# Performance work log

Hardware: AMD Instinct MI355X
Metric: run time of the kernel (lower is better)

Reference implementation:

```python
import jax, jax.numpy as jnp
import numpy as np


def setup_inputs() -> dict:
    key = jax.random.key(0)
    ks = jax.random.split(key, 9)
    V, D, C, B = 100000, 128, 10, 16384
    return {
        "target_w_id": jax.random.randint(ks[0], (B,), 0, V),
        "context_w_ids": jax.random.randint(ks[1], (B, C), 0, V),
        "R": jax.random.normal(ks[2], (V, D), dtype=jnp.float32),
        "M_w": jax.random.normal(ks[3], (2 * D, 2 * D), dtype=jnp.float32) * 0.05,
        "M_b": jax.random.normal(ks[4], (2 * D,), dtype=jnp.float32) * 0.05,
        "U_w": jax.random.normal(ks[5], (D, 2 * D), dtype=jnp.float32) * 0.05,
        "U_b": jax.random.normal(ks[6], (D,), dtype=jnp.float32) * 0.05,
        "W_w": jax.random.normal(ks[7], (D, 2 * D), dtype=jnp.float32) * 0.05,
        "W_b": jax.random.normal(ks[8], (D,), dtype=jnp.float32) * 0.05,
    }


def reference(target_w_id, context_w_ids, R, M_w, M_b, U_w, U_b, W_w, W_b):
    # Gather embeddings: tw [B, D], cw [B, C, D]
    tw = R[target_w_id]
    cw = R[context_w_ids]
    B, C, D = cw.shape
    # Concat context embed with (broadcast) target embed -> [B, C, 2D]
    tw_b = jnp.broadcast_to(tw[:, None, :], (B, C, D))
    stacked = jnp.concatenate([cw, tw_b], axis=-1)
    # Linear M (torch: x @ W.T + b), ReLU, sum over context window -> h [B, 2D]
    proj = jnp.einsum("bcd,ed->bce", stacked, M_w) + M_b
    h = jnp.sum(jax.nn.relu(proj), axis=1)
    posterior_mu = h @ U_w.T + U_b
    posterior_sigma = jax.nn.softplus(h @ W_w.T + W_b)
    return (posterior_mu, posterior_sigma)
```

## Files before the change

kernel.cpp:

```cpp
#include <hip/hip_runtime.h>
#include <hip/hip_bf16.h>

typedef __attribute__((ext_vector_type(8))) short short8;
typedef __attribute__((ext_vector_type(4))) float floatx4;
typedef __attribute__((ext_vector_type(2))) float floatx2;

static __device__ __forceinline__ short f2bf(float f) {
    union { float f; unsigned u; } v; v.f = f;
    unsigned r = v.u + 0x7fffu + ((v.u >> 16) & 1u);
    return (short)(r >> 16);
}
static __device__ __forceinline__ float bf2f(short s) {
    union { unsigned u; float f; } v; v.u = ((unsigned)(unsigned short)s) << 16;
    return v.f;
}

#define C_CTX 10
#define D_EMB 128
#define E_DIM 256


__global__ void prep_main(const float* __restrict__ Mw, const float* __restrict__ Uw,
                          const float* __restrict__ Ww, short* __restrict__ M1f,
                          short* __restrict__ M2f, short* __restrict__ B2f)
{
    int u = blockIdx.x * 256 + threadIdx.x;
    if (u < 8192) {
        int f = u & 4095;
        int l = f & 63, kc = (f >> 6) & 3, grp = f >> 8;
        int e = grp * 16 + (l & 15);
        int k = kc * 32 + (l >> 4) * 8 + ((u < 4096) ? 0 : 128);
        const float* src = Mw + (size_t)e * E_DIM + k;
        float4 x = *(const float4*)src;
        float4 y = *(const float4*)(src + 4);
        short8 o;
        o[0]=f2bf(x.x); o[1]=f2bf(x.y); o[2]=f2bf(x.z); o[3]=f2bf(x.w);
        o[4]=f2bf(y.x); o[5]=f2bf(y.y); o[6]=f2bf(y.z); o[7]=f2bf(y.w);
        *(short8*)(((u < 4096) ? M1f : M2f) + (size_t)f * 8) = o;
    } else {
        int f = u - 8192;
        int l = f & 63, ni = (f >> 6) & 3, kc = (f >> 8) & 7, w = f >> 11;
        int e = w * 64 + ni * 16 + (l & 15);
        const float* src = (e < 128) ? (Uw + (size_t)e * E_DIM)
                                     : (Ww + (size_t)(e - 128) * E_DIM);
        short8 o;
        #pragma unroll
        for (int i = 0; i < 8; ++i) {
            int pk = kc * 32 + (l >> 4) * 8 + i;
            int ok = (pk >> 6) * 64 + (pk & 3) * 16 + ((pk >> 2) & 15);
            o[i] = f2bf(src[ok]);
        }
        *(short8*)(B2f + (size_t)f * 8) = o;
    }
}

__global__ __launch_bounds__(256, 4)
void k_gt2(const float* __restrict__ R, const short* __restrict__ M1f,
           const short* __restrict__ M2f, const float* __restrict__ Mb,
           const int* __restrict__ tgt, unsigned char* __restrict__ G8,
           short* __restrict__ Ttb, int V, int NG)
{
    __shared__ __align__(16) short buf[1024 * 8];
    __shared__ int tids[64];
    const int t = threadIdx.x, w = t >> 6, l = t & 63;
    const bool isG = (int)blockIdx.x < NG;
    const int r0 = (isG ? blockIdx.x : (blockIdx.x - NG)) * 64;

    if (!isG && t < 64) tids[t] = tgt[r0 + t];
    if (!isG) __syncthreads();

    #pragma unroll
    for (int i = 0; i < 4; ++i) {
        int fa = t + i * 256;
        int li = fa & 63, frag = fa >> 6;
        int kc = frag >> 2, mi = frag & 3;
        int r = mi * 16 + (li & 15);
        int k = kc * 32 + (li >> 4) * 8;
        int gr;
        if (isG) { gr = r0 + r; if (gr >= V) gr = V - 1; }
        else     { gr = tids[r]; }
        const float* s = R + (size_t)gr * D_EMB + k;
        float4 x = *(const float4*)s;
        float4 y = *(const float4*)(s + 4);
        short8 v;
        v[0]=f2bf(x.x); v[1]=f2bf(x.y); v[2]=f2bf(x.z); v[3]=f2bf(x.w);
        v[4]=f2bf(y.x); v[5]=f2bf(y.y); v[6]=f2bf(y.z); v[7]=f2bf(y.w);
        *(short8*)&buf[fa * 8] = v;
    }
    __syncthreads();

    const short* Bf = isG ? M1f : M2f;
    floatx4 acc[4][4];
    #pragma unroll
    for (int mi = 0; mi < 4; ++mi)
        #pragma unroll
        for (int ni = 0; ni < 4; ++ni)
            acc[mi][ni] = (floatx4){0.f, 0.f, 0.f, 0.f};

    #pragma unroll
    for (int kc = 0; kc < 4; ++kc) {
        short8 afr[4], bfr[4];
        #pragma unroll
        for (int mi = 0; mi < 4; ++mi)
            afr[mi] = *(const short8*)&buf[((kc * 4 + mi) * 64 + l) * 8];
        #pragma unroll
        for (int ni = 0; ni < 4; ++ni)
            bfr[ni] = *(const short8*)(Bf + (((size_t)(w * 4 + ni) * 4 + kc) * 64 + l) * 8);
        #pragma unroll
        for (int mi = 0; mi < 4; ++mi)
            #pragma unroll
            for (int ni = 0; ni < 4; ++ni)
                acc[mi][ni] = __builtin_amdgcn_mfma_f32_16x16x32_bf16(afr[mi], bfr[ni], acc[mi][ni], 0, 0, 0);
    }

    const int pcb = w * 64 + (l & 15) * 4;
    if (isG) {
        #pragma unroll
        for (int mi = 0; mi < 4; ++mi)
            #pragma unroll
            for (int j = 0; j < 4; ++j) {
                int row = r0 + mi * 16 + (l >> 4) * 4 + j;
                if (row < V) {
                    int u = __builtin_amdgcn_cvt_pk_fp8_f32(acc[mi][0][j], acc[mi][1][j], 0, false);
                    u = __builtin_amdgcn_cvt_pk_fp8_f32(acc[mi][2][j], acc[mi][3][j], u, true);
                    *(int*)(G8 + (size_t)row * 256 + pcb) = u;
                }
            }
    } else {
        float mb[4];
        #pragma unroll
        for (int ni = 0; ni < 4; ++ni) mb[ni] = Mb[w * 64 + ni * 16 + (l & 15)];
        #pragma unroll
        for (int mi = 0; mi < 4; ++mi)
            #pragma unroll
            for (int j = 0; j < 4; ++j) {
                int row = r0 + mi * 16 + (l >> 4) * 4 + j;
                unsigned u0 = ((unsigned)(unsigned short)f2bf(acc[mi][1][j] + mb[1]) << 16)
                            |  (unsigned)(unsigned short)f2bf(acc[mi][0][j] + mb[0]);
                unsigned u1 = ((unsigned)(unsigned short)f2bf(acc[mi][3][j] + mb[3]) << 16)
                            |  (unsigned)(unsigned short)f2bf(acc[mi][2][j] + mb[2]);
                uint2 uv; uv.x = u0; uv.y = u1;
                *(uint2*)(Ttb + (size_t)row * 256 + pcb) = uv;
            }
    }
}

__global__ __launch_bounds__(256, 4)
void k_hh(const int* __restrict__ ctx, const unsigned char* __restrict__ G8,
          const short* __restrict__ Ttb, const short* __restrict__ B2f,
          const float* __restrict__ Ub, const float* __restrict__ Wb,
          float* __restrict__ out, int Bsz)
{
    __shared__ __align__(16) short hfr[8 * 64 * 8];
    __shared__ int ids[16 * C_CTX];
    const int t = threadIdx.x, w = t >> 6, l = t & 63;
    const int b0 = blockIdx.x * 16;

    if (t < 16 * C_CTX) ids[t] = ctx[(size_t)b0 * C_CTX + t];
    __syncthreads();

    const int hw = l >> 5;
    const int i5 = l & 31;
    const int kcc = i5 & 7, sub = i5 >> 3;
    const int c8 = kcc * 32 + sub * 8;

    #pragma unroll
    for (int p = 0; p < 2; ++p) {
        int bl = p * 8 + w * 2 + hw;
        short8 tr = *(const short8*)(Ttb + (size_t)(b0 + bl) * E_DIM + c8);
        float tv[8], acc[8];
        #pragma unroll
        for (int j = 0; j < 8; ++j) { tv[j] = bf2f(tr[j]); acc[j] = 0.f; }
        #pragma unroll
        for (int c = 0; c < C_CTX; ++c) {
            uint2 g = *(const uint2*)(G8 + (size_t)ids[bl * C_CTX + c] * E_DIM + c8);
            floatx2 d01 = __builtin_amdgcn_cvt_pk_f32_fp8((int)g.x, false);
            floatx2 d23 = __builtin_amdgcn_cvt_pk_f32_fp8((int)g.x, true);
            floatx2 d45 = __builtin_amdgcn_cvt_pk_f32_fp8((int)g.y, false);
            floatx2 d67 = __builtin_amdgcn_cvt_pk_f32_fp8((int)g.y, true);
            acc[0] += fmaxf(d01[0] + tv[0], 0.f);
            acc[1] += fmaxf(d01[1] + tv[1], 0.f);
            acc[2] += fmaxf(d23[0] + tv[2], 0.f);
            acc[3] += fmaxf(d23[1] + tv[3], 0.f);
            acc[4] += fmaxf(d45[0] + tv[4], 0.f);
            acc[5] += fmaxf(d45[1] + tv[5], 0.f);
            acc[6] += fmaxf(d67[0] + tv[6], 0.f);
            acc[7] += fmaxf(d67[1] + tv[7], 0.f);
        }
        int sp = (sub * 16 + bl) ^ kcc;
        short8 o;
        #pragma unroll
        for (int j = 0; j < 8; ++j) o[j] = f2bf(acc[j]);
        *(short8*)&hfr[(kcc * 64 + sp) * 8] = o;
    }
    __syncthreads();

    floatx4 acc2[4];
    #pragma unroll
    for (int ni = 0; ni < 4; ++ni)
        acc2[ni] = (floatx4){0.f, 0.f, 0.f, 0.f};

    #pragma unroll
    for (int kc = 0; kc < 8; ++kc) {
        short8 afr = *(const short8*)&hfr[(kc * 64 + (l ^ kc)) * 8];
        short8 bfr[4];
        #pragma unroll
        for (int ni = 0; ni < 4; ++ni)
            bfr[ni] = *(const short8*)(B2f + ((((size_t)w * 8 + kc) * 4 + ni) * 64 + l) * 8);
        #pragma unroll
        for (int ni = 0; ni < 4; ++ni)
            acc2[ni] = __builtin_amdgcn_mfma_f32_16x16x32_bf16(afr, bfr[ni], acc2[ni], 0, 0, 0);
    }

    #pragma unroll
    for (int ni = 0; ni < 4; ++ni) {
        int col = w * 64 + ni * 16 + (l & 15);
        #pragma unroll
        for (int j = 0; j < 4; ++j) {
            int rr = (l >> 4) * 4 + j;
            int r = b0 + rr;
            float v = acc2[ni][j];
            if (col < 128) {
                out[(size_t)r * 128 + col] = v + Ub[col];
            } else {
                float xx = v + Wb[col - 128];
                float sp = fmaxf(xx, 0.f) + log1pf(expf(-fabsf(xx)));
                out[(size_t)Bsz * 128 + (size_t)r * 128 + (col - 128)] = sp;
            }
        }
    }
}

extern "C" void kernel_launch(void* const* d_in, const int* in_sizes, int n_in,
                              void* d_out, int out_size, void* d_ws, size_t ws_size,
                              hipStream_t stream)
{
    const int*   tgt = (const int*)d_in[0];
    const int*   ctx = (const int*)d_in[1];
    const float* R   = (const float*)d_in[2];
    const float* Mw  = (const float*)d_in[3];
    const float* Mb  = (const float*)d_in[4];
    const float* Uw  = (const float*)d_in[5];
    const float* Ub  = (const float*)d_in[6];
    const float* Ww  = (const float*)d_in[7];
    const float* Wb  = (const float*)d_in[8];
    float* out = (float*)d_out;
    const int Bsz = in_sizes[0];
    const int Vn  = in_sizes[2] / D_EMB;

    char* ws = (char*)d_ws;
    size_t offG   = 0;
    size_t offT   = offG + (size_t)Vn * 256;
    size_t offM1f = offT + (size_t)Bsz * 512;
    size_t offM2f = offM1f + 65536;
    size_t offB2f = offM2f + 65536;

    unsigned char* G8 = (unsigned char*)(ws + offG);
    short* Ttb = (short*)(ws + offT);
    short* M1f = (short*)(ws + offM1f);
    short* M2f = (short*)(ws + offM2f);
    short* B2f = (short*)(ws + offB2f);

    const int NG = (Vn + 63) / 64;
    const int NT = Bsz / 64;

    prep_main<<<64, 256, 0, stream>>>(Mw, Uw, Ww, M1f, M2f, B2f);
    k_gt2<<<NG + NT, 256, 0, stream>>>(R, M1f, M2f, Mb, tgt, G8, Ttb, Vn, NG);
    k_hh<<<Bsz / 16, 256, 0, stream>>>(ctx, G8, Ttb, B2f, Ub, Wb, out, Bsz);
}
```

Before: 53.93 us.

## Double-buffer k_gt2 over two 64-row tiles to overlap loads with MFMA

Measured after the change: 53.32 us. About the same (-1.1%).

```diff
diff --git a/kernel.cpp b/kernel.cpp
--- a/kernel.cpp
+++ b/kernel.cpp
@@ -54,21 +54,11 @@
     }
 }
 
-__global__ __launch_bounds__(256, 4)
-void k_gt2(const float* __restrict__ R, const short* __restrict__ M1f,
-           const short* __restrict__ M2f, const float* __restrict__ Mb,
-           const int* __restrict__ tgt, unsigned char* __restrict__ G8,
-           short* __restrict__ Ttb, int V, int NG)
-{
-    __shared__ __align__(16) short buf[1024 * 8];
-    __shared__ int tids[64];
-    const int t = threadIdx.x, w = t >> 6, l = t & 63;
-    const bool isG = (int)blockIdx.x < NG;
-    const int r0 = (isG ? blockIdx.x : (blockIdx.x - NG)) * 64;
-
-    if (!isG && t < 64) tids[t] = tgt[r0 + t];
-    if (!isG) __syncthreads();
-
+struct Regs8 { float4 x[4]; float4 y[4]; };
+
+__device__ __forceinline__ void gt_load(const float* __restrict__ R, const int* tids_h,
+                                        bool isG, int r0h, int V, int t, Regs8& rg)
+{
     #pragma unroll
     for (int i = 0; i < 4; ++i) {
         int fa = t + i * 256;
@@ -77,19 +67,32 @@
         int r = mi * 16 + (li & 15);
         int k = kc * 32 + (li >> 4) * 8;
         int gr;
-        if (isG) { gr = r0 + r; if (gr >= V) gr = V - 1; }
-        else     { gr = tids[r]; }
+        if (isG) { gr = r0h + r; if (gr >= V) gr = V - 1; }
+        else     { gr = tids_h[r]; }
         const float* s = R + (size_t)gr * D_EMB + k;
-        float4 x = *(const float4*)s;
-        float4 y = *(const float4*)(s + 4);
+        rg.x[i] = *(const float4*)s;
+        rg.y[i] = *(const float4*)(s + 4);
+    }
+}
+
+__device__ __forceinline__ void gt_stage(short* bufh, int t, const Regs8& rg)
+{
+    #pragma unroll
+    for (int i = 0; i < 4; ++i) {
+        int fa = t + i * 256;
         short8 v;
-        v[0]=f2bf(x.x); v[1]=f2bf(x.y); v[2]=f2bf(x.z); v[3]=f2bf(x.w);
-        v[4]=f2bf(y.x); v[5]=f2bf(y.y); v[6]=f2bf(y.z); v[7]=f2bf(y.w);
-        *(short8*)&buf[fa * 8] = v;
-    }
-    __syncthreads();
-
-    const short* Bf = isG ? M1f : M2f;
+        v[0]=f2bf(rg.x[i].x); v[1]=f2bf(rg.x[i].y); v[2]=f2bf(rg.x[i].z); v[3]=f2bf(rg.x[i].w);
+        v[4]=f2bf(rg.y[i].x); v[5]=f2bf(rg.y[i].y); v[6]=f2bf(rg.y[i].z); v[7]=f2bf(rg.y[i].w);
+        *(short8*)&bufh[fa * 8] = v;
+    }
+}
+
+__device__ __forceinline__ void gt_compute(const short* bufh, const short* __restrict__ Bf,
+                                           const float* __restrict__ Mb, bool isG,
+                                           int r0h, int V, int w, int l,
+                                           unsigned char* __restrict__ G8,
+                                           short* __restrict__ Ttb)
+{
     floatx4 acc[4][4];
     #pragma unroll
     for (int mi = 0; mi < 4; ++mi)
@@ -102,7 +105,7 @@
         short8 afr[4], bfr[4];
         #pragma unroll
         for (int mi = 0; mi < 4; ++mi)
-            afr[mi] = *(const short8*)&buf[((kc * 4 + mi) * 64 + l) * 8];
+            afr[mi] = *(const short8*)&bufh[((kc * 4 + mi) * 64 + l) * 8];
         #pragma unroll
         for (int ni = 0; ni < 4; ++ni)
             bfr[ni] = *(const short8*)(Bf + (((size_t)(w * 4 + ni) * 4 + kc) * 64 + l) * 8);
@@ -119,7 +122,7 @@
         for (int mi = 0; mi < 4; ++mi)
             #pragma unroll
             for (int j = 0; j < 4; ++j) {
-                int row = r0 + mi * 16 + (l >> 4) * 4 + j;
+                int row = r0h + mi * 16 + (l >> 4) * 4 + j;
                 if (row < V) {
                     int u = __builtin_amdgcn_cvt_pk_fp8_f32(acc[mi][0][j], acc[mi][1][j], 0, false);
                     u = __builtin_amdgcn_cvt_pk_fp8_f32(acc[mi][2][j], acc[mi][3][j], u, true);
@@ -134,7 +137,7 @@
         for (int mi = 0; mi < 4; ++mi)
             #pragma unroll
             for (int j = 0; j < 4; ++j) {
-                int row = r0 + mi * 16 + (l >> 4) * 4 + j;
+                int row = r0h + mi * 16 + (l >> 4) * 4 + j;
                 unsigned u0 = ((unsigned)(unsigned short)f2bf(acc[mi][1][j] + mb[1]) << 16)
                             |  (unsigned)(unsigned short)f2bf(acc[mi][0][j] + mb[0]);
                 unsigned u1 = ((unsigned)(unsigned short)f2bf(acc[mi][3][j] + mb[3]) << 16)
@@ -145,7 +148,40 @@
     }
 }
 
-__global__ __launch_bounds__(256, 4)
+__global__ __launch_bounds__(256, 3)
+void k_gt2(const float* __restrict__ R, const short* __restrict__ M1f,
+           const short* __restrict__ M2f, const float* __restrict__ Mb,
+           const int* __restrict__ tgt, unsigned char* __restrict__ G8,
+           short* __restrict__ Ttb, int V, int NG)
+{
+    __shared__ __align__(16) short buf[2][1024 * 8];
+    __shared__ int tids[128];
+    const int t = threadIdx.x, w = t >> 6, l = t & 63;
+    const bool isG = (int)blockIdx.x < NG;
+    const int r0 = (isG ? blockIdx.x : (blockIdx.x - NG)) * 128;
+
+    if (!isG) {
+        if (t < 128) tids[t] = tgt[r0 + t];
+        __syncthreads();
+    }
+    const short* Bf = isG ? M1f : M2f;
+
+    Regs8 rg0;
+    gt_load(R, tids, isG, r0, V, t, rg0);
+    gt_stage(buf[0], t, rg0);
+    __syncthreads();
+
+    Regs8 rg1;
+    gt_load(R, tids + 64, isG, r0 + 64, V, t, rg1);
+
+    gt_compute(buf[0], Bf, Mb, isG, r0, V, w, l, G8, Ttb);
+
+    gt_stage(buf[1], t, rg1);
+    __syncthreads();
+    gt_compute(buf[1], Bf, Mb, isG, r0 + 64, V, w, l, G8, Ttb);
+}
+
+__global__ __launch_bounds__(256, 6)
 void k_hh(const int* __restrict__ ctx, const unsigned char* __restrict__ G8,
           const short* __restrict__ Ttb, const short* __restrict__ B2f,
           const float* __restrict__ Ub, const float* __restrict__ Wb,
@@ -261,8 +297,8 @@
     short* M2f = (short*)(ws + offM2f);
     short* B2f = (short*)(ws + offB2f);
 
-    const int NG = (Vn + 63) / 64;
-    const int NT = Bsz / 64;
+    const int NG = (Vn + 127) / 128;
+    const int NT = Bsz / 128;
 
     prep_main<<<64, 256, 0, stream>>>(Mw, Uw, Ww, M1f, M2f, B2f);
     k_gt2<<<NG + NT, 256, 0, stream>>>(R, M1f, M2f, Mb, tgt, G8, Ttb, Vn, NG);
```
